# Optimization experiments

Measured on AMD Instinct MI355X. Metric: run time of the kernel, lower is better.

The kernel has to match this reference:

```python
import jax, jax.numpy as jnp
import numpy as np

N = 50000      # nodes
E = 800000     # edges
DIN = 128      # in_channels
H = 128        # hidden_channels
G = 64         # graphs in batch
OUT = 8        # head out_channels


def setup_inputs() -> dict:
    key = jax.random.key(0)
    ks = jax.random.split(key, 12)
    s = 0.1  # weight init scale
    x = jax.random.normal(ks[0], (N, DIN), jnp.float32)
    edge_index = jax.random.randint(ks[1], (2, E), 0, N, dtype=jnp.int64)
    batch = jnp.sort(jax.random.randint(ks[2], (N,), 0, G, dtype=jnp.int64))
    W0 = jax.random.normal(ks[3], (DIN, H), jnp.float32) * s
    b0 = jnp.zeros((H,), jnp.float32)
    W1 = jax.random.normal(ks[4], (H, H), jnp.float32) * s
    b1 = jnp.zeros((H,), jnp.float32)
    W2 = jax.random.normal(ks[5], (H, H), jnp.float32) * s
    b2 = jnp.zeros((H,), jnp.float32)
    Wh = jax.random.normal(ks[6], (H, OUT), jnp.float32) * s
    bh = jnp.zeros((OUT,), jnp.float32)
    return {"x": x, "edge_index": edge_index, "batch": batch,
            "W0": W0, "b0": b0, "W1": W1, "b1": b1, "W2": W2, "b2": b2,
            "Wh": Wh, "bh": bh}


def gcn_conv(x, src, dst, W, b):
    # GCNConv with self-loops and symmetric normalization (PyG defaults).
    h = x @ W                                           # [N, H]
    deg = jnp.zeros((N,), h.dtype).at[dst].add(1.0) + 1.0   # in-degree incl. self-loop
    dinv = jax.lax.rsqrt(deg)                           # deg^{-1/2}
    coef = dinv[src] * dinv[dst]                        # [E]
    agg = jnp.zeros_like(h).at[dst].add(h[src] * coef[:, None])
    # self-loop contribution: dinv[i]^2 * h[i]
    return agg + h * (dinv * dinv)[:, None] + b


def reference(x, edge_index, batch, W0, b0, W1, b1, W2, b2, Wh, bh):
    src, dst = edge_index[0], edge_index[1]
    h = jax.nn.relu(gcn_conv(x, src, dst, W0, b0))
    h = jax.nn.relu(gcn_conv(h, src, dst, W1, b1))
    h = gcn_conv(h, src, dst, W2, b2)                   # last layer: no activation
    # global mean pool over graphs
    sums = jnp.zeros((G, H), h.dtype).at[batch].add(h)
    cnt = jnp.zeros((G,), h.dtype).at[batch].add(1.0)
    pooled = sums / jnp.maximum(cnt, 1.0)[:, None]      # [G, H]
    return pooled @ Wh + bh                             # [G, OUT]
```

## Files before the change

### kernel.cpp

```cpp
#include <hip/hip_runtime.h>

#define N_NODES 50000
#define N_EDGES 800000
#define HD 128
#define NGRAPH 64
#define NOUT 8
#define SLOTS 64
#define DSTRIDE 16

typedef __attribute__((ext_vector_type(8))) short bf8_t;
typedef __attribute__((ext_vector_type(4))) float f4_t;
typedef __attribute__((ext_vector_type(8))) unsigned short us8;

__device__ __forceinline__ unsigned short f2b(float f) {
    unsigned u = __float_as_uint(f);
    u += 0x7fffu + ((u >> 16) & 1u);
    return (unsigned short)(u >> 16);
}
__device__ __forceinline__ float b2f(unsigned short h) {
    return __uint_as_float(((unsigned)h) << 16);
}

__global__ __launch_bounds__(256) void fill1_k(const int* __restrict__ src,
                                               const int* __restrict__ dst,
                                               int* __restrict__ degc,
                                               unsigned short* __restrict__ slots) {
    int e = blockIdx.x * 256 + threadIdx.x;
    if (e >= N_EDGES) return;
    int s = __builtin_nontemporal_load(src + e);
    int d = __builtin_nontemporal_load(dst + e);
    int pos = atomicAdd(&degc[d * DSTRIDE], 1);
    if (pos < SLOTS)
        __builtin_nontemporal_store((unsigned short)s, &slots[(size_t)d * SLOTS + pos]);
}

__global__ __launch_bounds__(256) void cvtw_k(const float* __restrict__ W0,
                                              const float* __restrict__ W1,
                                              const float* __restrict__ W2,
                                              unsigned short* __restrict__ WT) {
    int idx = blockIdx.x * 256 + threadIdx.x;
    if (idx >= 3 * HD * HD) return;
    int w = idx >> 14;
    int rem = idx & 16383;
    int n = rem >> 7;
    int k = rem & 127;
    const float* W = (w == 0) ? W0 : (w == 1) ? W1 : W2;
    WT[(size_t)w * HD * HD + n * HD + k] = f2b(W[k * HD + n]);
}

__global__ __launch_bounds__(256) void mm_bf16_k(const unsigned short* __restrict__ X,
                                                 const unsigned short* __restrict__ WT,
                                                 const int* __restrict__ degc,
                                                 unsigned short* __restrict__ Y) {
    const int lane = threadIdx.x & 63;
    const int wave = threadIdx.x >> 6;
    const int r = lane & 15;
    const int q = lane >> 4;
    const int row0 = blockIdx.x * 64 + wave * 16;
    int arow = row0 + r; if (arow >= N_NODES) arow = N_NODES - 1;

    f4_t acc[8];
#pragma unroll
    for (int n = 0; n < 8; ++n) acc[n] = (f4_t){0.f, 0.f, 0.f, 0.f};

#pragma unroll
    for (int kb = 0; kb < 4; ++kb) {
        bf8_t a = *(const bf8_t*)(X + (size_t)arow * HD + kb * 32 + q * 8);
#pragma unroll
        for (int n = 0; n < 8; ++n) {
            bf8_t b = *(const bf8_t*)(WT + (size_t)(n * 16 + r) * HD + kb * 32 + q * 8);
            acc[n] = __builtin_amdgcn_mfma_f32_16x16x32_bf16(a, b, acc[n], 0, 0, 0);
        }
    }
    const int orow = row0 + q * 4;
#pragma unroll
    for (int i = 0; i < 4; ++i) {
        int rr = orow + i;
        if (rr < N_NODES) {
            float dv = rsqrtf((float)degc[rr * DSTRIDE] + 1.0f);
#pragma unroll
            for (int n = 0; n < 8; ++n)
                Y[(size_t)rr * HD + n * 16 + r] = f2b(acc[n][i] * dv);
        }
    }
}

__global__ __launch_bounds__(256) void mm_f32in_k(const float* __restrict__ X,
                                                  const unsigned short* __restrict__ WT,
                                                  const int* __restrict__ degc,
                                                  unsigned short* __restrict__ Y) {
    const int lane = threadIdx.x & 63;
    const int wave = threadIdx.x >> 6;
    const int r = lane & 15;
    const int q = lane >> 4;
    const int row0 = blockIdx.x * 64 + wave * 16;
    int arow = row0 + r; if (arow >= N_NODES) arow = N_NODES - 1;

    f4_t acc[8];
#pragma unroll
    for (int n = 0; n < 8; ++n) acc[n] = (f4_t){0.f, 0.f, 0.f, 0.f};

#pragma unroll
    for (int kb = 0; kb < 4; ++kb) {
        float4 fa = *(const float4*)(X + (size_t)arow * HD + kb * 32 + q * 8);
        float4 fb = *(const float4*)(X + (size_t)arow * HD + kb * 32 + q * 8 + 4);
        bf8_t a;
        a[0] = (short)f2b(fa.x); a[1] = (short)f2b(fa.y);
        a[2] = (short)f2b(fa.z); a[3] = (short)f2b(fa.w);
        a[4] = (short)f2b(fb.x); a[5] = (short)f2b(fb.y);
        a[6] = (short)f2b(fb.z); a[7] = (short)f2b(fb.w);
#pragma unroll
        for (int n = 0; n < 8; ++n) {
            bf8_t b = *(const bf8_t*)(WT + (size_t)(n * 16 + r) * HD + kb * 32 + q * 8);
            acc[n] = __builtin_amdgcn_mfma_f32_16x16x32_bf16(a, b, acc[n], 0, 0, 0);
        }
    }
    const int orow = row0 + q * 4;
#pragma unroll
    for (int i = 0; i < 4; ++i) {
        int rr = orow + i;
        if (rr < N_NODES) {
            float dv = rsqrtf((float)degc[rr * DSTRIDE] + 1.0f);
#pragma unroll
            for (int n = 0; n < 8; ++n)
                Y[(size_t)rr * HD + n * 16 + r] = f2b(acc[n][i] * dv);
        }
    }
}

__global__ __launch_bounds__(256) void gather_k(const unsigned short* __restrict__ T,
                                                const int* __restrict__ degc,
                                                const unsigned short* __restrict__ slots,
                                                const float* __restrict__ b,
                                                unsigned short* __restrict__ out,
                                                int relu) {
    int i = blockIdx.x * 16 + (threadIdx.x >> 4);
    if (i >= N_NODES) return;
    const int j8 = (threadIdx.x & 15) * 8;
    const int dg = degc[i * DSTRIDE];
    int dc = dg; if (dc > SLOTS) dc = SLOTS;
    const float di = rsqrtf((float)dg + 1.0f);
    const unsigned short* sl = slots + (size_t)i * SLOTS;

    float a[8];
#pragma unroll
    for (int k = 0; k < 8; ++k) a[k] = 0.f;

    int e = 0;
    for (; e + 15 < dc; e += 16) {
        int s[16];
#pragma unroll
        for (int u = 0; u < 16; ++u) s[u] = sl[e + u];
        us8 v[16];
#pragma unroll
        for (int u = 0; u < 16; ++u) v[u] = *(const us8*)(T + (size_t)s[u] * HD + j8);
#pragma unroll
        for (int u = 0; u < 16; ++u) {
#pragma unroll
            for (int k = 0; k < 8; ++k) a[k] += b2f(v[u][k]);
        }
    }
    for (; e + 7 < dc; e += 8) {
        int s[8];
#pragma unroll
        for (int u = 0; u < 8; ++u) s[u] = sl[e + u];
        us8 v[8];
#pragma unroll
        for (int u = 0; u < 8; ++u) v[u] = *(const us8*)(T + (size_t)s[u] * HD + j8);
#pragma unroll
        for (int u = 0; u < 8; ++u) {
#pragma unroll
            for (int k = 0; k < 8; ++k) a[k] += b2f(v[u][k]);
        }
    }
    for (; e < dc; ++e) {
        int s = sl[e];
        us8 v = *(const us8*)(T + (size_t)s * HD + j8);
#pragma unroll
        for (int k = 0; k < 8; ++k) a[k] += b2f(v[k]);
    }
    us8 tv = *(const us8*)(T + (size_t)i * HD + j8);
    float4 bv0 = *(const float4*)(b + j8);
    float4 bv1 = *(const float4*)(b + j8 + 4);
    float bb[8] = {bv0.x, bv0.y, bv0.z, bv0.w, bv1.x, bv1.y, bv1.z, bv1.w};
    us8 o;
#pragma unroll
    for (int k = 0; k < 8; ++k) {
        float r = di * (a[k] + b2f(tv[k])) + bb[k];
        if (relu) r = fmaxf(r, 0.f);
        o[k] = f2b(r);
    }
    *(us8*)(out + (size_t)i * HD + j8) = o;
}

__global__ __launch_bounds__(256) void pool2_k(const unsigned short* __restrict__ H2,
                                               const int* __restrict__ batch,
                                               float* __restrict__ sums,
                                               float* __restrict__ cnt) {
    const int t = threadIdx.x;
    const int f = t & 127;
    const int half = t >> 7;
    int i0 = blockIdx.x * 128 + half * 64;
    if (i0 >= N_NODES) return;
    int i1 = i0 + 64; if (i1 > N_NODES) i1 = N_NODES;

    int cur = batch[i0];
    float acc = 0.f;
    float c = 0.f;
    for (int i = i0; i < i1; ++i) {
        int g = batch[i];
        if (g != cur) {
            atomicAdd(&sums[cur * HD + f], acc);
            if (f == 0) atomicAdd(&cnt[cur], c);
            acc = 0.f; c = 0.f; cur = g;
        }
        acc += b2f(H2[(size_t)i * HD + f]);
        c += 1.f;
    }
    atomicAdd(&sums[cur * HD + f], acc);
    if (f == 0) atomicAdd(&cnt[cur], c);
}

__global__ __launch_bounds__(512) void head_k(const float* __restrict__ sums,
                                              const float* __restrict__ cnt,
                                              const float* __restrict__ Wh,
                                              const float* __restrict__ bh,
                                              float* __restrict__ out) {
    int t = threadIdx.x;
    int g = t >> 3, o = t & 7;
    float inv = 1.0f / fmaxf(cnt[g], 1.0f);
    float acc = bh[o];
    for (int h = 0; h < HD; ++h)
        acc += sums[g * HD + h] * inv * Wh[h * NOUT + o];
    out[g * NOUT + o] = acc;
}

extern "C" void kernel_launch(void* const* d_in, const int* in_sizes, int n_in,
                              void* d_out, int out_size, void* d_ws, size_t ws_size,
                              hipStream_t stream) {
    const float* x  = (const float*)d_in[0];
    const int*   ei = (const int*)d_in[1];
    const int*   batch = (const int*)d_in[2];
    const float* W0 = (const float*)d_in[3];
    const float* b0 = (const float*)d_in[4];
    const float* W1 = (const float*)d_in[5];
    const float* b1 = (const float*)d_in[6];
    const float* W2 = (const float*)d_in[7];
    const float* b2 = (const float*)d_in[8];
    const float* Wh = (const float*)d_in[9];
    const float* bh = (const float*)d_in[10];
    float* out = (float*)d_out;

    const int* src = ei;
    const int* dst = ei + N_EDGES;

    char* wsb = (char*)d_ws;
    int*            degc  = (int*)(wsb + 0);
    unsigned short* slots = (unsigned short*)(wsb + 3200000);
    unsigned short* WT    = (unsigned short*)(wsb + 9600000);
    unsigned short* A     = (unsigned short*)(wsb + 9698304);
    unsigned short* B     = (unsigned short*)(wsb + 22498304);
    float*          sums  = (float*)(wsb + 35298304);
    float*          cnt   = (float*)(wsb + 35331072);

    const int mmGrid = (N_NODES + 63) / 64;
    const int gaGrid = (N_NODES + 15) / 16;

    hipMemsetAsync(degc, 0, (size_t)N_NODES * DSTRIDE * sizeof(int), stream);
    fill1_k<<<(N_EDGES + 255) / 256, 256, 0, stream>>>(src, dst, degc, slots);
    cvtw_k<<<(3 * HD * HD + 255) / 256, 256, 0, stream>>>(W0, W1, W2, WT);

    mm_f32in_k<<<mmGrid, 256, 0, stream>>>(x, WT, degc, A);
    gather_k<<<gaGrid, 256, 0, stream>>>(A, degc, slots, b0, B, 1);

    mm_bf16_k<<<mmGrid, 256, 0, stream>>>(B, WT + HD * HD, degc, A);
    gather_k<<<gaGrid, 256, 0, stream>>>(A, degc, slots, b1, B, 1);

    mm_bf16_k<<<mmGrid, 256, 0, stream>>>(B, WT + 2 * HD * HD, degc, A);
    gather_k<<<gaGrid, 256, 0, stream>>>(A, degc, slots, b2, B, 0);

    hipMemsetAsync(sums, 0, (NGRAPH * HD + NGRAPH) * sizeof(float), stream);
    pool2_k<<<(N_NODES + 127) / 128, 256, 0, stream>>>(B, batch, sums, cnt);
    head_k<<<1, 512, 0, stream>>>(sums, cnt, Wh, bh, out);
}
```

Baseline: 349.7 us.

## Fuse gather-aggregate with next layer GEMM via shared memory; unpad degree counters

Layers 0 and 1 now aggregate neighbours and apply bias and ReLU straight into a shared-memory tile of 64 rows, which feeds the next layer's MFMA matmul in the same kernel. This removes a write and re-read of the intermediate activations and two kernel launches. The degree counter array also loses its 16-int padding stride, shrinking the memset and making reads contiguous, though atomics on neighbouring counters may now contend on shared cache lines. Each fused block handles 64 rows with 16 threads per row, so gather parallelism per block drops and occupancy may fall because of the shared-memory tile.

```diff
diff --git a/kernel.cpp b/kernel.cpp
--- a/kernel.cpp
+++ b/kernel.cpp
@@ -6,7 +6,6 @@
 #define NGRAPH 64
 #define NOUT 8
 #define SLOTS 64
-#define DSTRIDE 16
 
 typedef __attribute__((ext_vector_type(8))) short bf8_t;
 typedef __attribute__((ext_vector_type(4))) float f4_t;
@@ -29,7 +28,7 @@
     if (e >= N_EDGES) return;
     int s = __builtin_nontemporal_load(src + e);
     int d = __builtin_nontemporal_load(dst + e);
-    int pos = atomicAdd(&degc[d * DSTRIDE], 1);
+    int pos = atomicAdd(&degc[d], 1);
     if (pos < SLOTS)
         __builtin_nontemporal_store((unsigned short)s, &slots[(size_t)d * SLOTS + pos]);
 }
@@ -48,43 +47,6 @@
     WT[(size_t)w * HD * HD + n * HD + k] = f2b(W[k * HD + n]);
 }
 
-__global__ __launch_bounds__(256) void mm_bf16_k(const unsigned short* __restrict__ X,
-                                                 const unsigned short* __restrict__ WT,
-                                                 const int* __restrict__ degc,
-                                                 unsigned short* __restrict__ Y) {
-    const int lane = threadIdx.x & 63;
-    const int wave = threadIdx.x >> 6;
-    const int r = lane & 15;
-    const int q = lane >> 4;
-    const int row0 = blockIdx.x * 64 + wave * 16;
-    int arow = row0 + r; if (arow >= N_NODES) arow = N_NODES - 1;
-
-    f4_t acc[8];
-#pragma unroll
-    for (int n = 0; n < 8; ++n) acc[n] = (f4_t){0.f, 0.f, 0.f, 0.f};
-
-#pragma unroll
-    for (int kb = 0; kb < 4; ++kb) {
-        bf8_t a = *(const bf8_t*)(X + (size_t)arow * HD + kb * 32 + q * 8);
-#pragma unroll
-        for (int n = 0; n < 8; ++n) {
-            bf8_t b = *(const bf8_t*)(WT + (size_t)(n * 16 + r) * HD + kb * 32 + q * 8);
-            acc[n] = __builtin_amdgcn_mfma_f32_16x16x32_bf16(a, b, acc[n], 0, 0, 0);
-        }
-    }
-    const int orow = row0 + q * 4;
-#pragma unroll
-    for (int i = 0; i < 4; ++i) {
-        int rr = orow + i;
-        if (rr < N_NODES) {
-            float dv = rsqrtf((float)degc[rr * DSTRIDE] + 1.0f);
-#pragma unroll
-            for (int n = 0; n < 8; ++n)
-                Y[(size_t)rr * HD + n * 16 + r] = f2b(acc[n][i] * dv);
-        }
-    }
-}
-
 __global__ __launch_bounds__(256) void mm_f32in_k(const float* __restrict__ X,
                                                   const unsigned short* __restrict__ WT,
                                                   const int* __restrict__ degc,
@@ -120,10 +82,115 @@
     for (int i = 0; i < 4; ++i) {
         int rr = orow + i;
         if (rr < N_NODES) {
-            float dv = rsqrtf((float)degc[rr * DSTRIDE] + 1.0f);
+            float dv = rsqrtf((float)degc[rr] + 1.0f);
 #pragma unroll
             for (int n = 0; n < 8; ++n)
                 Y[(size_t)rr * HD + n * 16 + r] = f2b(acc[n][i] * dv);
+        }
+    }
+}
+
+__global__ __launch_bounds__(256) void fusedGM_k(const unsigned short* __restrict__ T,
+                                                 const int* __restrict__ degc,
+                                                 const unsigned short* __restrict__ slots,
+                                                 const float* __restrict__ bias,
+                                                 const unsigned short* __restrict__ WT,
+                                                 unsigned short* __restrict__ Y) {
+    __shared__ unsigned short hs[64][136];
+    const int tid = threadIdx.x;
+    const int base = blockIdx.x * 64;
+
+    {
+        const int g = tid >> 4;
+        const int l = tid & 15;
+        const int j8 = l * 8;
+        float4 bv0 = *(const float4*)(bias + j8);
+        float4 bv1 = *(const float4*)(bias + j8 + 4);
+        float bb[8] = {bv0.x, bv0.y, bv0.z, bv0.w, bv1.x, bv1.y, bv1.z, bv1.w};
+        for (int ii = 0; ii < 4; ++ii) {
+            const int lrow = g * 4 + ii;
+            int i = base + lrow; if (i >= N_NODES) i = N_NODES - 1;
+            const int dg = degc[i];
+            int dc = dg; if (dc > SLOTS) dc = SLOTS;
+            const float di = rsqrtf((float)dg + 1.0f);
+            const unsigned short* sl = slots + (size_t)i * SLOTS;
+
+            float a[8];
+#pragma unroll
+            for (int k = 0; k < 8; ++k) a[k] = 0.f;
+            int e = 0;
+            for (; e + 15 < dc; e += 16) {
+                int s[16];
+#pragma unroll
+                for (int u = 0; u < 16; ++u) s[u] = sl[e + u];
+                us8 v[16];
+#pragma unroll
+                for (int u = 0; u < 16; ++u) v[u] = *(const us8*)(T + (size_t)s[u] * HD + j8);
+#pragma unroll
+                for (int u = 0; u < 16; ++u) {
+#pragma unroll
+                    for (int k = 0; k < 8; ++k) a[k] += b2f(v[u][k]);
+                }
+            }
+            for (; e + 7 < dc; e += 8) {
+                int s[8];
+#pragma unroll
+                for (int u = 0; u < 8; ++u) s[u] = sl[e + u];
+                us8 v[8];
+#pragma unroll
+                for (int u = 0; u < 8; ++u) v[u] = *(const us8*)(T + (size_t)s[u] * HD + j8);
+#pragma unroll
+                for (int u = 0; u < 8; ++u) {
+#pragma unroll
+                    for (int k = 0; k < 8; ++k) a[k] += b2f(v[u][k]);
+                }
+            }
+            for (; e < dc; ++e) {
+                int s = sl[e];
+                us8 v = *(const us8*)(T + (size_t)s * HD + j8);
+#pragma unroll
+                for (int k = 0; k < 8; ++k) a[k] += b2f(v[k]);
+            }
+            us8 tv = *(const us8*)(T + (size_t)i * HD + j8);
+            us8 o;
+#pragma unroll
+            for (int k = 0; k < 8; ++k) {
+                float r = di * (a[k] + b2f(tv[k])) + bb[k];
+                r = fmaxf(r, 0.f);
+                o[k] = f2b(r);
+            }
+            *(us8*)(&hs[lrow][j8]) = o;
+        }
+    }
+    __syncthreads();
+
+    {
+        const int lane = tid & 63;
+        const int wave = tid >> 6;
+        const int r = lane & 15;
+        const int q = lane >> 4;
+        f4_t acc[8];
+#pragma unroll
+        for (int n = 0; n < 8; ++n) acc[n] = (f4_t){0.f, 0.f, 0.f, 0.f};
+#pragma unroll
+        for (int kb = 0; kb < 4; ++kb) {
+            bf8_t a = *(const bf8_t*)(&hs[wave * 16 + r][kb * 32 + q * 8]);
+#pragma unroll
+            for (int n = 0; n < 8; ++n) {
+                bf8_t b = *(const bf8_t*)(WT + (size_t)(n * 16 + r) * HD + kb * 32 + q * 8);
+                acc[n] = __builtin_amdgcn_mfma_f32_16x16x32_bf16(a, b, acc[n], 0, 0, 0);
+            }
+        }
+        const int orow = base + wave * 16 + q * 4;
+#pragma unroll
+        for (int i = 0; i < 4; ++i) {
+            int rr = orow + i;
+            if (rr < N_NODES) {
+                float dv = rsqrtf((float)degc[rr] + 1.0f);
+#pragma unroll
+                for (int n = 0; n < 8; ++n)
+                    Y[(size_t)rr * HD + n * 16 + r] = f2b(acc[n][i] * dv);
+            }
         }
     }
 }
@@ -132,12 +199,11 @@
                                                 const int* __restrict__ degc,
                                                 const unsigned short* __restrict__ slots,
                                                 const float* __restrict__ b,
-                                                unsigned short* __restrict__ out,
-                                                int relu) {
+                                                unsigned short* __restrict__ out) {
     int i = blockIdx.x * 16 + (threadIdx.x >> 4);
     if (i >= N_NODES) return;
     const int j8 = (threadIdx.x & 15) * 8;
-    const int dg = degc[i * DSTRIDE];
+    const int dg = degc[i];
     int dc = dg; if (dc > SLOTS) dc = SLOTS;
     const float di = rsqrtf((float)dg + 1.0f);
     const unsigned short* sl = slots + (size_t)i * SLOTS;
@@ -145,7 +211,6 @@
     float a[8];
 #pragma unroll
     for (int k = 0; k < 8; ++k) a[k] = 0.f;
-
     int e = 0;
     for (; e + 15 < dc; e += 16) {
         int s[16];
@@ -185,11 +250,8 @@
     float bb[8] = {bv0.x, bv0.y, bv0.z, bv0.w, bv1.x, bv1.y, bv1.z, bv1.w};
     us8 o;
 #pragma unroll
-    for (int k = 0; k < 8; ++k) {
-        float r = di * (a[k] + b2f(tv[k])) + bb[k];
-        if (relu) r = fmaxf(r, 0.f);
-        o[k] = f2b(r);
-    }
+    for (int k = 0; k < 8; ++k)
+        o[k] = f2b(di * (a[k] + b2f(tv[k])) + bb[k]);
     *(us8*)(out + (size_t)i * HD + j8) = o;
 }
 
@@ -256,30 +318,29 @@
 
     char* wsb = (char*)d_ws;
     int*            degc  = (int*)(wsb + 0);
-    unsigned short* slots = (unsigned short*)(wsb + 3200000);
-    unsigned short* WT    = (unsigned short*)(wsb + 9600000);
-    unsigned short* A     = (unsigned short*)(wsb + 9698304);
-    unsigned short* B     = (unsigned short*)(wsb + 22498304);
-    float*          sums  = (float*)(wsb + 35298304);
-    float*          cnt   = (float*)(wsb + 35331072);
+    unsigned short* slots = (unsigned short*)(wsb + 200000);
+    unsigned short* WT    = (unsigned short*)(wsb + 6600000);
+    unsigned short* A     = (unsigned short*)(wsb + 6698304);
+    unsigned short* C     = (unsigned short*)(wsb + 19498304);
+    float*          sums  = (float*)(wsb + 32298304);
+    float*          cnt   = (float*)(wsb + 32331072);
 
     const int mmGrid = (N_NODES + 63) / 64;
     const int gaGrid = (N_NODES + 15) / 16;
 
-    hipMemsetAsync(degc, 0, (size_t)N_NODES * DSTRIDE * sizeof(int), stream);
+    hipMemsetAsync(degc, 0, N_NODES * sizeof(int), stream);
     fill1_k<<<(N_EDGES + 255) / 256, 256, 0, stream>>>(src, dst, degc, slots);
     cvtw_k<<<(3 * HD * HD + 255) / 256, 256, 0, stream>>>(W0, W1, W2, WT);
 
     mm_f32in_k<<<mmGrid, 256, 0, stream>>>(x, WT, degc, A);
-    gather_k<<<gaGrid, 256, 0, stream>>>(A, degc, slots, b0, B, 1);
-
-    mm_bf16_k<<<mmGrid, 256, 0, stream>>>(B, WT + HD * HD, degc, A);
-    gather_k<<<gaGrid, 256, 0, stream>>>(A, degc, slots, b1, B, 1);
-
-    mm_bf16_k<<<mmGrid, 256, 0, stream>>>(B, WT + 2 * HD * HD, degc, A);
-    gather_k<<<gaGrid, 256, 0, stream>>>(A, degc, slots, b2, B, 0);
+
+    fusedGM_k<<<mmGrid, 256, 0, stream>>>(A, degc, slots, b0, WT + HD * HD, C);
+
+    fusedGM_k<<<mmGrid, 256, 0, stream>>>(C, degc, slots, b1, WT + 2 * HD * HD, A);
+
+    gather_k<<<gaGrid, 256, 0, stream>>>(A, degc, slots, b2, C);
 
     hipMemsetAsync(sums, 0, (NGRAPH * HD + NGRAPH) * sizeof(float), stream);
-    pool2_k<<<(N_NODES + 127) / 128, 256, 0, stream>>>(B, batch, sums, cnt);
+    pool2_k<<<(N_NODES + 127) / 128, 256, 0, stream>>>(C, batch, sums, cnt);
     head_k<<<1, 512, 0, stream>>>(sums, cnt, Wh, bh, out);
 }
```

After: 383.6 us. 9.7% more time.
